# Kernel optimization log

Hardware: AMD Instinct MI355X
Metric: run time of the kernel (lower is better)

## Reference

```python
import math
import jax, jax.numpy as jnp
import numpy as np

B, T, C, H, DQK, DV = 2, 2048, 1024, 16, 64, 64


def setup_inputs() -> dict:
    key = jax.random.key(0)
    ks = jax.random.split(key, 5)
    x = jax.random.normal(ks[0], (B, T, C), dtype=jnp.float32)
    # randw: randn(*d) / sqrt(d[-1])
    w_q = jax.random.normal(ks[1], (H, DQK, C), dtype=jnp.float32) / math.sqrt(C)
    w_k = jax.random.normal(ks[2], (H, DQK, C), dtype=jnp.float32) / math.sqrt(C)
    w_v = jax.random.normal(ks[3], (H, DV, C), dtype=jnp.float32) / math.sqrt(C)
    w_o = jax.random.normal(ks[4], (DV * H, C), dtype=jnp.float32) / math.sqrt(C)
    return {"x": x, "w_q": w_q, "w_k": w_k, "w_v": w_v, "w_o": w_o}


def reference(x, w_q, w_k, w_v, w_o):
    # Full-sequence causal forward (bs_q.first == 0, nb == T): caches are
    # fully written in one shot, so they reduce to the plain projections.
    n, t, c = x.shape
    q = jnp.einsum('ntc,hdc->nhtd', x, w_q)
    k = jnp.einsum('ntc,hdc->nhtd', x, w_k)
    v = jnp.einsum('ntc,hdc->nhtd', x, w_v)
    scale = 1.0 / math.sqrt(w_q.shape[1])
    a = jnp.einsum('nhtd,nhsd->nhts', q, k) * scale  # [n,h,t,s]
    causal = jnp.arange(t)[:, None] < jnp.arange(t)[None, :]  # True above diag
    a = jnp.where(causal[None, None, :, :], -jnp.inf, a)
    a = jax.nn.softmax(a, axis=3)
    y = jnp.einsum('nhts,nhsd->nthd', a, v).reshape(n, t, -1)  # [n,t,h*dv]
    return y @ w_o  # cache_y, [n,t,c]
```

## Files before the change

kernel.cpp:

```cpp
#include <hip/hip_runtime.h>


typedef short bf16x4 __attribute__((ext_vector_type(4)));
typedef short bf16x8 __attribute__((ext_vector_type(8)));
typedef float f32x4 __attribute__((ext_vector_type(4)));

#define MFMA_BF16 __builtin_amdgcn_mfma_f32_16x16x32_bf16

#define QSCALE 0.18033688011112042f

__device__ __forceinline__ unsigned short f2bf(float f) {
    union { float f; unsigned u; } un; un.f = f;
    unsigned r = un.u + 0x7fffu + ((un.u >> 16) & 1u);
    return (unsigned short)(r >> 16);
}
__device__ __forceinline__ unsigned pk2(float a, float b) {
    return (unsigned)f2bf(a) | ((unsigned)f2bf(b) << 16);
}
__device__ __forceinline__ unsigned pk2t(float a, float b) {
    union { float f; unsigned u; } ua, ub; ua.f = a; ub.f = b;
    return __builtin_amdgcn_perm(ub.u, ua.u, 0x07060302u);
}
__device__ __forceinline__ void gload16(const void* g, void* l) {
    __builtin_amdgcn_global_load_lds(
        (const __attribute__((address_space(1))) unsigned int*)g,
        (__attribute__((address_space(3))) unsigned int*)l, 16, 0, 0);
}

__global__ __launch_bounds__(256) void prep(
    const float* __restrict__ x, const float* __restrict__ wq,
    const float* __restrict__ wk, const float* __restrict__ wv,
    const float* __restrict__ wo,
    unsigned short* __restrict__ x16, unsigned short* __restrict__ wq16,
    unsigned short* __restrict__ wk16, unsigned short* __restrict__ wv16,
    unsigned short* __restrict__ wot)
{
    const int bid = blockIdx.x;
    if (bid < 3584) {
        const float* s; unsigned short* d; int off;
        if (bid < 2048)      { s = x;  d = x16;  off = bid * 2048; }
        else if (bid < 2560) { s = wq; d = wq16; off = (bid - 2048) * 2048; }
        else if (bid < 3072) { s = wk; d = wk16; off = (bid - 2560) * 2048; }
        else                 { s = wv; d = wv16; off = (bid - 3072) * 2048; }
        int i = off + threadIdx.x * 8;
        float4 f0 = *(const float4*)&s[i], f1 = *(const float4*)&s[i + 4];
        uint4 o;
        o.x = pk2(f0.x, f0.y); o.y = pk2(f0.z, f0.w);
        o.z = pk2(f1.x, f1.y); o.w = pk2(f1.z, f1.w);
        *(uint4*)&d[i] = o;
    } else {
        __shared__ unsigned short t[64 * 72];
        const int b2 = bid - 3584;
        const int k0 = (b2 & 15) << 6, n0 = (b2 >> 4) << 6;
        const int r = threadIdx.x >> 2, cg = (threadIdx.x & 3) << 4;
        const float* src = &wo[(k0 + r) * 1024 + n0 + cg];
        #pragma unroll
        for (int j = 0; j < 16; j += 4) {
            float4 f = *(const float4*)&src[j];
            t[(cg + j + 0) * 72 + r] = f2bf(f.x);
            t[(cg + j + 1) * 72 + r] = f2bf(f.y);
            t[(cg + j + 2) * 72 + r] = f2bf(f.z);
            t[(cg + j + 3) * 72 + r] = f2bf(f.w);
        }
        __syncthreads();
        unsigned short* dst = &wot[(n0 + r) * 1024 + k0 + cg];
        unsigned short* tr = &t[r * 72 + cg];
        unsigned v[16];
        #pragma unroll
        for (int j = 0; j < 16; ++j) v[j] = tr[j];
        uint4 o0, o1;
        o0.x = v[0] | (v[1] << 16);   o0.y = v[2] | (v[3] << 16);
        o0.z = v[4] | (v[5] << 16);   o0.w = v[6] | (v[7] << 16);
        o1.x = v[8] | (v[9] << 16);   o1.y = v[10] | (v[11] << 16);
        o1.z = v[12] | (v[13] << 16); o1.w = v[14] | (v[15] << 16);
        *(uint4*)&dst[0] = o0;
        *(uint4*)&dst[8] = o1;
    }
}

template<int MODE, int KCNT>
__device__ __forceinline__ void gemm_body(
    const unsigned short* __restrict__ A, const unsigned short* __restrict__ Bm,
    void* __restrict__ C, int m0, int n0, int ldc, float sc, int kbase,
    unsigned short* sa, unsigned short* sb)
{
    const int tid = threadIdx.x, wave = tid >> 6, lane = tid & 63;
    const int l15 = lane & 15, l4 = lane >> 4;
    const int wm = (wave >> 1) << 6, wn = (wave & 1) << 6;

    const int r16 = lane >> 2;
    const int gcol = (((lane & 3) ^ ((r16 >> 1) & 3)) << 3);
    const int rcol = (l4 ^ ((l15 >> 1) & 3)) << 3;
    const unsigned short* Ag0 = &A[(size_t)(m0 + wave * 16 + r16) * 1024 + kbase + gcol];
    const unsigned short* Ag1 = Ag0 + (size_t)64 * 1024;
    const unsigned short* Bg0 = &Bm[(size_t)(n0 + wave * 16 + r16) * 1024 + kbase + gcol];
    const unsigned short* Bg1 = Bg0 + (size_t)64 * 1024;
    const int lb0 = (wave * 16) * 32;
    const int lb1 = (64 + wave * 16) * 32;

    gload16(Ag0, &sa[lb0]);
    gload16(Ag1, &sa[lb1]);
    gload16(Bg0, &sb[lb0]);
    gload16(Bg1, &sb[lb1]);
    __syncthreads();

    f32x4 acc[4][4] = {};

    #pragma unroll
    for (int kk = 0; kk < KCNT; ++kk) {
        const int cb = (kk & 1) * 4096;
        if (kk < KCNT - 1) {
            const int off = (kk + 1) * 32;
            const int nb2 = 4096 - cb;
            gload16(Ag0 + off, &sa[nb2 + lb0]);
            gload16(Ag1 + off, &sa[nb2 + lb1]);
            gload16(Bg0 + off, &sb[nb2 + lb0]);
            gload16(Bg1 + off, &sb[nb2 + lb1]);
        }
        bf16x8 af[4], bf4[4];
        #pragma unroll
        for (int i = 0; i < 4; ++i)
            af[i] = *(const bf16x8*)&sa[cb + (wm + i * 16 + l15) * 32 + rcol];
        #pragma unroll
        for (int j = 0; j < 4; ++j)
            bf4[j] = *(const bf16x8*)&sb[cb + (wn + j * 16 + l15) * 32 + rcol];
        #pragma unroll
        for (int i = 0; i < 4; ++i)
            #pragma unroll
            for (int j = 0; j < 4; ++j)
                acc[i][j] = MFMA_BF16(af[i], bf4[j], acc[i][j], 0, 0, 0);
        __syncthreads();
    }

    #pragma unroll
    for (int i = 0; i < 4; ++i)
        #pragma unroll
        for (int j = 0; j < 4; ++j)
            #pragma unroll
            for (int r = 0; r < 4; ++r) {
                int row = m0 + wm + i * 16 + l4 * 4 + r;
                int col = n0 + wn + j * 16 + l15;
                float val = acc[i][j][r];
                if (MODE == 0) {
                    int nb = row >> 11, t = row & 2047;
                    int hh = col >> 6, dd = col & 63;
                    ((unsigned short*)C)[(((nb << 4) + hh) * 2048 + t) * 64 + dd] =
                        f2bf(val * sc);
                } else if (MODE == 1) {
                    ((float*)C)[(size_t)row * ldc + col] = val;
                } else {
                    int s = col & 31;
                    int cp = (col & ~31) | (((s >> 2) & 3) << 3)
                                         | (((s >> 4) & 1) << 2) | (s & 3);
                    ((unsigned short*)C)[(size_t)row * ldc + cp] = f2bf(val);
                }
            }
}

__global__ __launch_bounds__(256) void proj(
    const unsigned short* __restrict__ x16,
    const unsigned short* __restrict__ wq16,
    const unsigned short* __restrict__ wk16,
    const unsigned short* __restrict__ wv16,
    unsigned short* __restrict__ qbuf,
    unsigned short* __restrict__ kbuf,
    unsigned short* __restrict__ vtb)
{
    __shared__ unsigned short sa[2 * 128 * 32];
    __shared__ unsigned short sb[2 * 128 * 32];
    const int bid = blockIdx.x;
    if (bid < 512) {
        int m0 = (bid & 31) << 7;
        int n0g = (bid >> 5) << 7;
        if (n0g < 1024)
            gemm_body<0, 32>(x16, wq16, qbuf, m0, n0g, 0, QSCALE, 0, sa, sb);
        else
            gemm_body<0, 32>(x16, wk16, kbuf, m0, n0g - 1024, 0, 1.0f, 0, sa, sb);
    } else {
        int v = bid - 512;
        gemm_body<2, 32>(wv16, x16, vtb, (v & 7) << 7, (v >> 3) << 7, 4096, 1.0f, 0, sa, sb);
    }
}

__global__ __launch_bounds__(256) void outp(
    const unsigned short* __restrict__ ybuf,
    const unsigned short* __restrict__ wot,
    float* __restrict__ out)
{
    __shared__ unsigned short sa[2 * 128 * 32];
    __shared__ unsigned short sb[2 * 128 * 32];
    const int bid = blockIdx.x;
    gemm_body<1, 32>(ybuf, wot, out, (bid & 31) << 7, (bid >> 5) << 7,
                     1024, 1.0f, 0, sa, sb);
}

__global__ __launch_bounds__(512, 2) void attn(
    const unsigned short* __restrict__ q,
    const unsigned short* __restrict__ k,
    const unsigned short* __restrict__ vt,
    unsigned short* __restrict__ y)
{
    __shared__ unsigned short sk[2][2][64 * 64];
    __shared__ unsigned short sv[2][2][64 * 64];
    const int tid = threadIdx.x, wave = tid >> 6, lane = tid & 63;
    const int ws = wave & 3, wk2 = wave >> 2;
    const int l15 = lane & 15, l4 = lane >> 4;
    const int bid = blockIdx.x;
    const int pr = bid >> 5;
    const int bh = bid & 31;
    const int nb = bh >> 4, hh = bh & 15;
    const size_t base = (size_t)bh << 17;

    const int lrow = lane >> 3;
    const int gch = ((lane & 7) ^ lrow) << 3;
    const int row = wave * 8 + lrow;
    const unsigned short* kg = &k[base + (size_t)row * 64 + gch];
    const unsigned short* vg = &vt[(size_t)((hh << 6) + row) * 4096 + (nb << 11) + gch];
    const int lb = (wave * 8) * 64;

    const int rch0 = ((0 + l4) ^ (l15 & 7)) << 3;
    const int rch1 = ((4 + l4) ^ (l15 & 7)) << 3;

    float* mrg = (float*)&sk[0][0][0];
    float* lsr = (float*)&sv[0][0][0];
    const int mslot = (ws << 6) + lane;
    const int mb = mslot << 5;

    auto process = [&](const int t) {
        const int q0 = t << 7;
        bf16x8 qf[2][2];
        #pragma unroll
        for (int g = 0; g < 2; ++g)
            #pragma unroll
            for (int ks = 0; ks < 2; ++ks)
                qf[g][ks] = *(const bf16x8*)
                    &q[base + (size_t)(q0 + (g << 6) + ws * 16 + l15) * 64 + ks * 32 + l4 * 8];

        float l_sum[2] = {0.f, 0.f};
        f32x4 acc[2][4] = {};
        const int nsup = t + 1;

        auto stage_pair = [&](const int sbuf, const int p) {
            gload16(kg + ((size_t)p << 13),        &sk[sbuf][0][lb]);
            gload16(kg + ((size_t)p << 13) + 4096, &sk[sbuf][1][lb]);
            gload16(vg + (p << 7),      &sv[sbuf][0][lb]);
            gload16(vg + (p << 7) + 64, &sv[sbuf][1][lb]);
        };

        stage_pair(0, 0);
        __syncthreads();

        auto sstep = [&](const int cur, const int p) {
            if (p + 1 < nsup) stage_pair(cur ^ 1, p + 1);
            const int st = 2 * p + wk2;
            const unsigned short* skc = &sk[cur][wk2][0];
            const unsigned short* svc = &sv[cur][wk2][0];

            f32x4 s_acc[2][4] = {};
            __builtin_amdgcn_s_setprio(1);
            #pragma unroll
            for (int ns = 0; ns < 4; ++ns) {
                bf16x8 kf0 = *(const bf16x8*)&skc[(ns * 16 + l15) * 64 + rch0];
                bf16x8 kf1 = *(const bf16x8*)&skc[(ns * 16 + l15) * 64 + rch1];
                s_acc[0][ns] = MFMA_BF16(kf0, qf[0][0], s_acc[0][ns], 0, 0, 0);
                s_acc[0][ns] = MFMA_BF16(kf1, qf[0][1], s_acc[0][ns], 0, 0, 0);
                s_acc[1][ns] = MFMA_BF16(kf0, qf[1][0], s_acc[1][ns], 0, 0, 0);
                s_acc[1][ns] = MFMA_BF16(kf1, qf[1][1], s_acc[1][ns], 0, 0, 0);
            }
            __builtin_amdgcn_s_setprio(0);

            if (p == nsup - 1) {
                const int sb = st << 6;
                #pragma unroll
                for (int g = 0; g < 2; ++g) {
                    const int qlg = q0 + (g << 6) + ws * 16 + l15;
                    #pragma unroll
                    for (int ns = 0; ns < 4; ++ns)
                        #pragma unroll
                        for (int r = 0; r < 4; ++r)
                            if (sb + ns * 16 + l4 * 4 + r > qlg) s_acc[g][ns][r] = -1e30f;
                }
            }

            float pe[2][4][4];
            #pragma unroll
            for (int g = 0; g < 2; ++g)
                #pragma unroll
                for (int ns = 0; ns < 4; ++ns) {
                    #pragma unroll
                    for (int r = 0; r < 4; ++r) pe[g][ns][r] = exp2f(s_acc[g][ns][r]);
                    l_sum[g] += (pe[g][ns][0] + pe[g][ns][1]) + (pe[g][ns][2] + pe[g][ns][3]);
                }

            #pragma unroll
            for (int ks = 0; ks < 2; ++ks) {
                bf16x8 pf0, pf1;
                {
                    uint4 pw;
                    pw.x = pk2t(pe[0][2 * ks][0], pe[0][2 * ks][1]);
                    pw.y = pk2t(pe[0][2 * ks][2], pe[0][2 * ks][3]);
                    pw.z = pk2t(pe[0][2 * ks + 1][0], pe[0][2 * ks + 1][1]);
                    pw.w = pk2t(pe[0][2 * ks + 1][2], pe[0][2 * ks + 1][3]);
                    pf0 = *(bf16x8*)&pw;
                }
                {
                    uint4 pw;
                    pw.x = pk2t(pe[1][2 * ks][0], pe[1][2 * ks][1]);
                    pw.y = pk2t(pe[1][2 * ks][2], pe[1][2 * ks][3]);
                    pw.z = pk2t(pe[1][2 * ks + 1][0], pe[1][2 * ks + 1][1]);
                    pw.w = pk2t(pe[1][2 * ks + 1][2], pe[1][2 * ks + 1][3]);
                    pf1 = *(bf16x8*)&pw;
                }
                const int rch = ks ? rch1 : rch0;
                __builtin_amdgcn_s_setprio(1);
                #pragma unroll
                for (int ds = 0; ds < 4; ++ds) {
                    bf16x8 vf = *(const bf16x8*)&svc[(ds * 16 + l15) * 64 + rch];
                    acc[0][ds] = MFMA_BF16(vf, pf0, acc[0][ds], 0, 0, 0);
                    acc[1][ds] = MFMA_BF16(vf, pf1, acc[1][ds], 0, 0, 0);
                }
                __builtin_amdgcn_s_setprio(0);
            }
            __syncthreads();
        };

        int p = 0;
        for (; p + 2 <= nsup; p += 2) { sstep(0, p); sstep(1, p + 1); }
        if (p < nsup) sstep(0, p);

        if (wk2 == 1) {
            #pragma unroll
            for (int g = 0; g < 2; ++g)
                #pragma unroll
                for (int ds = 0; ds < 4; ++ds) {
                    const int c = g * 4 + ds;
                    *(f32x4*)&mrg[mb + ((c ^ (lane & 7)) << 2)] = acc[g][ds];
                }
            lsr[(mslot << 1) + 0] = l_sum[0];
            lsr[(mslot << 1) + 1] = l_sum[1];
        }
        __syncthreads();
        if (wk2 == 0) {
            #pragma unroll
            for (int g = 0; g < 2; ++g)
                #pragma unroll
                for (int ds = 0; ds < 4; ++ds) {
                    const int c = g * 4 + ds;
                    acc[g][ds] += *(const f32x4*)&mrg[mb + ((c ^ (lane & 7)) << 2)];
                }
            l_sum[0] += lsr[(mslot << 1) + 0];
            l_sum[1] += lsr[(mslot << 1) + 1];

            #pragma unroll
            for (int g = 0; g < 2; ++g) {
                float ls = l_sum[g];
                ls += __shfl_xor(ls, 16);
                ls += __shfl_xor(ls, 32);
                const float rl = __builtin_amdgcn_rcpf(ls);

                const size_t rowbase =
                    ((size_t)((nb << 11) + q0 + (g << 6) + ws * 16 + l15) << 10) + (hh << 6) + l4 * 4;
                #pragma unroll
                for (int ds = 0; ds < 4; ++ds) {
                    uint2 o;
                    o.x = pk2(acc[g][ds][0] * rl, acc[g][ds][1] * rl);
                    o.y = pk2(acc[g][ds][2] * rl, acc[g][ds][3] * rl);
                    *(uint2*)&y[rowbase + ds * 16] = o;
                }
            }
        }
        __syncthreads();
    };

    process(15 - pr);
    process(pr);
}

extern "C" void kernel_launch(void* const* d_in, const int* in_sizes, int n_in,
                              void* d_out, int out_size, void* d_ws, size_t ws_size,
                              hipStream_t stream) {
    const float* x  = (const float*)d_in[0];
    const float* wq = (const float*)d_in[1];
    const float* wk = (const float*)d_in[2];
    const float* wv = (const float*)d_in[3];
    const float* wo = (const float*)d_in[4];
    float* out = (float*)d_out;

    const size_t M1 = 1u << 20;
    unsigned short* x16  = (unsigned short*)d_ws;
    unsigned short* wq16 = x16 + 4 * M1;
    unsigned short* wk16 = wq16 + M1;
    unsigned short* wv16 = wk16 + M1;
    unsigned short* wot  = wv16 + M1;
    unsigned short* qbuf = wot + M1;
    unsigned short* kbuf = qbuf + 4 * M1;
    unsigned short* vtb  = kbuf + 4 * M1;
    unsigned short* ybuf = vtb + 4 * M1;

    dim3 blk(256);
    prep<<<3840, blk, 0, stream>>>(x, wq, wk, wv, wo, x16, wq16, wk16, wv16, wot);
    proj<<<768, blk, 0, stream>>>(x16, wq16, wk16, wv16, qbuf, kbuf, vtb);
    attn<<<256, dim3(512), 0, stream>>>(qbuf, kbuf, vtb, ybuf);
    outp<<<256, blk, 0, stream>>>(ybuf, wot, out);
}
```

Baseline: 170.3 us.

## Rewrite output projection GEMM with 512-thread blocks and dedicated double-buffered loop

Replaces the shared gemm_body call in the output projection with a specialised kernel that uses 8 waves per 128x128 tile, each computing a 32x64 sub-tile. It double-buffers K-slices of 32 through LDS with async global-to-LDS loads and XOR-swizzled columns. The goal is more waves per block to hide latency and fewer accumulators per wave. The trade-off is one block barrier per K step and direct per-element fp32 stores in the epilogue.

Measured after the change: 172.8 us. No clear change (+1.4%).

```diff
diff --git a/kernel.cpp b/kernel.cpp
--- a/kernel.cpp
+++ b/kernel.cpp
@@ -182,16 +182,67 @@
     }
 }
 
-__global__ __launch_bounds__(256) void outp(
+__global__ __launch_bounds__(512) void outp(
     const unsigned short* __restrict__ ybuf,
     const unsigned short* __restrict__ wot,
     float* __restrict__ out)
 {
-    __shared__ unsigned short sa[2 * 128 * 32];
-    __shared__ unsigned short sb[2 * 128 * 32];
+    __shared__ unsigned short sa[2 * 4096];
+    __shared__ unsigned short sb[2 * 4096];
+    const int tid = threadIdx.x, wave = tid >> 6, lane = tid & 63;
+    const int l15 = lane & 15, l4 = lane >> 4;
+    const int wm = (wave >> 1) << 5;
+    const int wn = (wave & 1) << 6;
     const int bid = blockIdx.x;
-    gemm_body<1, 32>(ybuf, wot, out, (bid & 31) << 7, (bid >> 5) << 7,
-                     1024, 1.0f, 0, sa, sb);
+    const int m0 = (bid & 31) << 7, n0 = (bid >> 5) << 7;
+
+    const int r16 = lane >> 2;
+    const int gcol = (((lane & 3) ^ ((r16 >> 1) & 3)) << 3);
+    const int rcol = (l4 ^ ((l15 >> 1) & 3)) << 3;
+    const unsigned short* Ag = &ybuf[(size_t)(m0 + wave * 16 + r16) * 1024 + gcol];
+    const unsigned short* Bg = &wot[(size_t)(n0 + wave * 16 + r16) * 1024 + gcol];
+    const int lb = (wave * 16) * 32;
+
+    gload16(Ag, &sa[lb]);
+    gload16(Bg, &sb[lb]);
+    __syncthreads();
+
+    f32x4 acc[2][4] = {};
+
+    #pragma unroll
+    for (int kk = 0; kk < 32; ++kk) {
+        const int cb = (kk & 1) * 4096;
+        if (kk < 31) {
+            const int off = (kk + 1) * 32;
+            const int nb2 = 4096 - cb;
+            gload16(Ag + off, &sa[nb2 + lb]);
+            gload16(Bg + off, &sb[nb2 + lb]);
+        }
+        bf16x8 af[2], bf4[4];
+        #pragma unroll
+        for (int i = 0; i < 2; ++i)
+            af[i] = *(const bf16x8*)&sa[cb + (wm + i * 16 + l15) * 32 + rcol];
+        #pragma unroll
+        for (int j = 0; j < 4; ++j)
+            bf4[j] = *(const bf16x8*)&sb[cb + (wn + j * 16 + l15) * 32 + rcol];
+        #pragma unroll
+        for (int i = 0; i < 2; ++i)
+            #pragma unroll
+            for (int j = 0; j < 4; ++j)
+                acc[i][j] = MFMA_BF16(af[i], bf4[j], acc[i][j], 0, 0, 0);
+        __syncthreads();
+    }
+
+    #pragma unroll
+    for (int i = 0; i < 2; ++i)
+        #pragma unroll
+        for (int j = 0; j < 4; ++j)
+            #pragma unroll
+            for (int r = 0; r < 4; ++r) {
+                int row = m0 + wm + i * 16 + l4 * 4 + r;
+                int col = n0 + wn + j * 16 + l15;
+                out[(size_t)row * 1024 + col] = acc[i][j][r];
+            }
 }
 
 __global__ __launch_bounds__(512, 2) void attn(
@@ -401,5 +452,5 @@
     prep<<<3840, blk, 0, stream>>>(x, wq, wk, wv, wo, x16, wq16, wk16, wv16, wot);
     proj<<<768, blk, 0, stream>>>(x16, wq16, wk16, wv16, qbuf, kbuf, vtb);
     attn<<<256, dim3(512), 0, stream>>>(qbuf, kbuf, vtb, ybuf);
-    outp<<<256, blk, 0, stream>>>(ybuf, wot, out);
-}
+    outp<<<256, dim3(512), 0, stream>>>(ybuf, wot, out);
+}
```
